# Performance work log

Measured on AMD Instinct MI355X. Metric: run time of the kernel, lower is better.

Reference implementation:

```python
import jax, jax.numpy as jnp
import numpy as np

B, D, C, S = 65536, 128, 10, 2
LAMBDA_E, LAMBDA_OD = 0.1, 0.036
GAMMA_E, GAMMA_OD = 2.0, 2.0
STEP_SIZE = 1000.0


def setup_inputs() -> dict:
    key = jax.random.key(0)
    ks = jax.random.split(key, 12)
    inp = {
        "mean_t": jax.random.normal(ks[0], (B, D), jnp.float32),
        "mean_s": jax.random.normal(ks[1], (B, D), jnp.float32),
        "log_std_t": jax.random.normal(ks[2], (B, D), jnp.float32),
        "log_std_s": jax.random.normal(ks[3], (B, D), jnp.float32),
        "y_zt": jax.random.normal(ks[4], (B, C), jnp.float32),
        "s_zt": jax.random.normal(ks[5], (B, S), jnp.float32),
        "eps_prior_t": jax.random.normal(ks[6], (B, D), jnp.float32),
        "eps_prior_s": jax.random.normal(ks[7], (B, D), jnp.float32),
        "eps_t": jax.random.normal(ks[8], (B, D), jnp.float32),
        "eps_s": jax.random.normal(ks[9], (B, D), jnp.float32),
        "target": jax.random.randint(ks[10], (B,), 0, C, jnp.int64),
        "current_step": 500,
    }
    return inp


def _kld_batchmean(log_p, t):
    # torch KLDivLoss(reduction='batchmean'): sum(t * (log t - log_p)) / batch
    return jnp.sum(t * (jnp.log(t) - log_p)) / t.shape[0]


def reference(mean_t, mean_s, log_std_t, log_std_s, y_zt, s_zt,
              eps_prior_t, eps_prior_s, eps_t, eps_s, target, current_step):
    # CIFAR10 branch: cross entropy on task logits
    logp_y = jax.nn.log_softmax(y_zt, axis=1)
    L_t = -jnp.mean(jnp.take_along_axis(logp_y, target[:, None], axis=1))

    # entropy loss on sensitive discriminator output
    sm = jax.nn.softmax(s_zt, axis=1)
    lsm = jax.nn.log_softmax(s_zt, axis=1)
    Loss_e = -jnp.sum(sm * lsm) / s_zt.shape[0]

    # prior samples: N(0, I) and N(1, I)  (mean_tensors(zeros, ones))
    prior_t = eps_prior_t            # mean 0
    prior_s = 1.0 + eps_prior_s      # mean 1

    # encoder samples: MVN(mean, diag(exp(log_std))) -> std = exp(0.5*log_std)
    # torch .sample() is non-differentiable -> stop_gradient
    enc_t = jax.lax.stop_gradient(mean_t + jnp.exp(0.5 * log_std_t) * eps_t)
    enc_s = jax.lax.stop_gradient(mean_s + jnp.exp(0.5 * log_std_s) * eps_s)

    L_zt = _kld_batchmean(jax.nn.log_softmax(prior_t, axis=1), jax.nn.softmax(enc_t, axis=1))
    L_zs = _kld_batchmean(jax.nn.log_softmax(prior_s, axis=1), jax.nn.softmax(enc_s, axis=1))

    frac = current_step / STEP_SIZE
    lam_e = LAMBDA_E * GAMMA_E ** frac
    lam_od = LAMBDA_OD * GAMMA_OD ** frac
    return L_t + lam_e * Loss_e + lam_od * (L_zt + L_zs)
```

## Files before the change

### kernel.cpp

```cpp
#include <hip/hip_runtime.h>
#include <hip/hip_bf16.h>
#include <math.h>

#define BATCH   65536
#define NCLS    10
#define NBLOCKS 2048
#define PAIRS   4

typedef float vf4 __attribute__((ext_vector_type(4)));


__global__ __launch_bounds__(256, 4) void crit_main(
    const float* __restrict__ mean_t,      const float* __restrict__ mean_s,
    const float* __restrict__ log_std_t,   const float* __restrict__ log_std_s,
    const float* __restrict__ y_zt,        const float* __restrict__ s_zt,
    const float* __restrict__ eps_prior_t, const float* __restrict__ eps_prior_s,
    const float* __restrict__ eps_t,       const float* __restrict__ eps_s,
    const int*   __restrict__ target,
    double*      __restrict__ ws_partial)
{
    const int tid  = threadIdx.x;
    const int lane = tid & 63;
    const int sub  = lane & 31;
    const int half = lane >> 5;
    const int gwave = blockIdx.x * 4 + (tid >> 6);
    const int base  = gwave * PAIRS;

    const vf4* MT = (const vf4*)mean_t;
    const vf4* LT = (const vf4*)log_std_t;
    const vf4* ET = (const vf4*)eps_t;
    const vf4* PT = (const vf4*)eps_prior_t;
    const vf4* MS = (const vf4*)mean_s;
    const vf4* LS = (const vf4*)log_std_s;
    const vf4* ES = (const vf4*)eps_s;
    const vf4* PS = (const vf4*)eps_prior_s;

    int    tgt[PAIRS];
    float2 y0[PAIRS], y1[PAIRS], y2[PAIRS], y3[PAIRS], y4[PAIRS], s2[PAIRS];
    if (sub == 0) {
        #pragma unroll
        for (int i = 0; i < PAIRS; ++i) {
            const int r = (base + i) * 2 + half;
            tgt[i] = target[r];
            const float* yr = y_zt + (size_t)r * NCLS;
            y0[i] = *(const float2*)(yr + 0);
            y1[i] = *(const float2*)(yr + 2);
            y2[i] = *(const float2*)(yr + 4);
            y3[i] = *(const float2*)(yr + 6);
            y4[i] = *(const float2*)(yr + 8);
            s2[i] = *(const float2*)(s_zt + (size_t)r * 2);
        }
    }

    float part[PAIRS][6];
    #pragma unroll
    for (int i = 0; i < PAIRS; ++i) {
        const int fidx = (base + i) * 64 + lane;

        const vf4 mu_t = __builtin_nontemporal_load(&MT[fidx]);
        const vf4 ls_t = __builtin_nontemporal_load(&LT[fidx]);
        const vf4 ep_t = __builtin_nontemporal_load(&ET[fidx]);
        const vf4 pr_t = __builtin_nontemporal_load(&PT[fidx]);
        const vf4 mu_s = __builtin_nontemporal_load(&MS[fidx]);
        const vf4 ls_s = __builtin_nontemporal_load(&LS[fidx]);
        const vf4 ep_s = __builtin_nontemporal_load(&ES[fidx]);
        const vf4 pr_s = __builtin_nontemporal_load(&PS[fidx]);

        const float et0 = fmaf(__expf(0.5f * ls_t.x), ep_t.x, mu_t.x);
        const float et1 = fmaf(__expf(0.5f * ls_t.y), ep_t.y, mu_t.y);
        const float et2 = fmaf(__expf(0.5f * ls_t.z), ep_t.z, mu_t.z);
        const float et3 = fmaf(__expf(0.5f * ls_t.w), ep_t.w, mu_t.w);
        const float es0 = fmaf(__expf(0.5f * ls_s.x), ep_s.x, mu_s.x);
        const float es1 = fmaf(__expf(0.5f * ls_s.y), ep_s.y, mu_s.y);
        const float es2 = fmaf(__expf(0.5f * ls_s.z), ep_s.z, mu_s.z);
        const float es3 = fmaf(__expf(0.5f * ls_s.w), ep_s.w, mu_s.w);

        const float xt0 = __expf(et0), xt1 = __expf(et1);
        const float xt2 = __expf(et2), xt3 = __expf(et3);
        const float xs0 = __expf(es0), xs1 = __expf(es1);
        const float xs2 = __expf(es2), xs3 = __expf(es3);

        part[i][0] = (xt0 + xt1) + (xt2 + xt3);
        part[i][1] = (__expf(pr_t.x) + __expf(pr_t.y)) + (__expf(pr_t.z) + __expf(pr_t.w));
        part[i][2] = (xt0 * (et0 - pr_t.x) + xt1 * (et1 - pr_t.y))
                   + (xt2 * (et2 - pr_t.z) + xt3 * (et3 - pr_t.w));
        part[i][3] = (xs0 + xs1) + (xs2 + xs3);
        part[i][4] = (__expf(pr_s.x) + __expf(pr_s.y)) + (__expf(pr_s.z) + __expf(pr_s.w));
        part[i][5] = (xs0 * (es0 - pr_s.x) + xs1 * (es1 - pr_s.y))
                   + (xs2 * (es2 - pr_s.z) + xs3 * (es3 - pr_s.w));
    }

    #pragma unroll
    for (int m = 16; m >= 1; m >>= 1) {
        #pragma unroll
        for (int i = 0; i < PAIRS; ++i) {
            #pragma unroll
            for (int j = 0; j < 6; ++j) part[i][j] += __shfl_xor(part[i][j], m, 64);
        }
    }

    float kl_sum = 0.0f, ce_sum = 0.0f, H_sum = 0.0f;
    #pragma unroll
    for (int i = 0; i < PAIRS; ++i) {
        const float rt = 1.0f / part[i][0];
        const float rs = 1.0f / part[i][3];
        kl_sum += part[i][2] * rt + __logf(part[i][1] * rt)
                + part[i][5] * rs + __logf(part[i][4] * rs);
    }
    if (sub == 0) {
        #pragma unroll
        for (int i = 0; i < PAIRS; ++i) {
            const int t = tgt[i];
            float yt = y0[i].x;
            yt = (t == 1) ? y0[i].y : yt;
            yt = (t == 2) ? y1[i].x : yt;
            yt = (t == 3) ? y1[i].y : yt;
            yt = (t == 4) ? y2[i].x : yt;
            yt = (t == 5) ? y2[i].y : yt;
            yt = (t == 6) ? y3[i].x : yt;
            yt = (t == 7) ? y3[i].y : yt;
            yt = (t == 8) ? y4[i].x : yt;
            yt = (t == 9) ? y4[i].y : yt;

            const float Z = (__expf(y0[i].x) + __expf(y0[i].y))
                          + (__expf(y1[i].x) + __expf(y1[i].y))
                          + (__expf(y2[i].x) + __expf(y2[i].y))
                          + (__expf(y3[i].x) + __expf(y3[i].y))
                          + (__expf(y4[i].x) + __expf(y4[i].y));
            ce_sum += __logf(Z) - yt;

            const float za = __expf(s2[i].x), zb = __expf(s2[i].y);
            const float Zs = za + zb;
            const float lses = __logf(Zs);
            H_sum += -((za / Zs) * (s2[i].x - lses) + (zb / Zs) * (s2[i].y - lses));
        }
    }

    __shared__ double sh[8][3];
    if (sub == 0) {
        const int slot = tid >> 5;
        sh[slot][0] = (double)ce_sum;
        sh[slot][1] = (double)H_sum;
        sh[slot][2] = (double)kl_sum;
    }
    __syncthreads();
    if (tid == 0) {
        double c = 0.0, h = 0.0, k = 0.0;
        #pragma unroll
        for (int i = 0; i < 8; ++i) { c += sh[i][0]; h += sh[i][1]; k += sh[i][2]; }
        ws_partial[blockIdx.x * 3 + 0] = c;
        ws_partial[blockIdx.x * 3 + 1] = h;
        ws_partial[blockIdx.x * 3 + 2] = k;
    }
}

__global__ __launch_bounds__(256) void crit_reduce(
    const double* __restrict__ ws_partial,
    const int*    __restrict__ step_ptr,
    float*        __restrict__ out,
    int nblocks)
{
    const int tid = threadIdx.x;
    double c = 0.0, h = 0.0, k = 0.0;
    for (int i = tid; i < nblocks; i += 256) {
        c += ws_partial[3 * i + 0];
        h += ws_partial[3 * i + 1];
        k += ws_partial[3 * i + 2];
    }
    __shared__ double sc[256], sh_[256], sk[256];
    sc[tid] = c; sh_[tid] = h; sk[tid] = k;
    __syncthreads();
    for (int s = 128; s > 0; s >>= 1) {
        if (tid < s) { sc[tid] += sc[tid + s]; sh_[tid] += sh_[tid + s]; sk[tid] += sk[tid + s]; }
        __syncthreads();
    }
    if (tid == 0) {
        double frac  = (double)step_ptr[0] / 1000.0;
        double lam_e  = 0.1   * exp2(frac);
        double lam_od = 0.036 * exp2(frac);
        out[0] = (float)((sc[0] + lam_e * sh_[0] + lam_od * sk[0]) / (double)BATCH);
    }
}

extern "C" void kernel_launch(void* const* d_in, const int* in_sizes, int n_in,
                              void* d_out, int out_size, void* d_ws, size_t ws_size,
                              hipStream_t stream) {
    const float* mean_t      = (const float*)d_in[0];
    const float* mean_s      = (const float*)d_in[1];
    const float* log_std_t   = (const float*)d_in[2];
    const float* log_std_s   = (const float*)d_in[3];
    const float* y_zt        = (const float*)d_in[4];
    const float* s_zt        = (const float*)d_in[5];
    const float* eps_prior_t = (const float*)d_in[6];
    const float* eps_prior_s = (const float*)d_in[7];
    const float* eps_t       = (const float*)d_in[8];
    const float* eps_s       = (const float*)d_in[9];
    const int*   target      = (const int*)d_in[10];
    const int*   step_ptr    = (const int*)d_in[11];

    double* ws_partial = (double*)d_ws;
    float*  out        = (float*)d_out;

    crit_main<<<NBLOCKS, 256, 0, stream>>>(
        mean_t, mean_s, log_std_t, log_std_s, y_zt, s_zt,
        eps_prior_t, eps_prior_s, eps_t, eps_s, target, ws_partial);
    crit_reduce<<<1, 256, 0, stream>>>(ws_partial, step_ptr, out, NBLOCKS);
}
```

Baseline: 243.2 us.

## Split CE/entropy work into dedicated blocks and remap KL rows to 16-lane groups

The per-row cross-entropy and entropy work moves out of the KL blocks into 64 extra dedicated blocks, where every thread handles four rows instead of one lane per half-wave doing it serially. In the KL blocks, each 16-lane group now handles one row with two vf4 loads per tensor, giving 8 rows per wave and a 4-step shuffle reduction instead of 5. The aim is to drop the serialized scalar y_zt/s_zt/target loads and lane divergence from the bandwidth-bound KL path. In exchange, the block reduction becomes a full 256-entry double shared-memory tree with more barriers, and the y_zt row accesses in the new blocks are strided by 40 bytes.

```diff
diff --git a/kernel.cpp b/kernel.cpp
--- a/kernel.cpp
+++ b/kernel.cpp
@@ -2,10 +2,11 @@
 #include <hip/hip_bf16.h>
 #include <math.h>
 
-#define BATCH   65536
-#define NCLS    10
-#define NBLOCKS 2048
-#define PAIRS   4
+#define BATCH 65536
+#define NCLS  10
+#define NKL   2048
+#define NCE   64
+#define NBTOT (NKL + NCE)
 
 typedef float vf4 __attribute__((ext_vector_type(4)));
 
@@ -19,138 +20,140 @@
     const int*   __restrict__ target,
     double*      __restrict__ ws_partial)
 {
-    const int tid  = threadIdx.x;
-    const int lane = tid & 63;
-    const int sub  = lane & 31;
-    const int half = lane >> 5;
-    const int gwave = blockIdx.x * 4 + (tid >> 6);
-    const int base  = gwave * PAIRS;
-
-    const vf4* MT = (const vf4*)mean_t;
-    const vf4* LT = (const vf4*)log_std_t;
-    const vf4* ET = (const vf4*)eps_t;
-    const vf4* PT = (const vf4*)eps_prior_t;
-    const vf4* MS = (const vf4*)mean_s;
-    const vf4* LS = (const vf4*)log_std_s;
-    const vf4* ES = (const vf4*)eps_s;
-    const vf4* PS = (const vf4*)eps_prior_s;
-
-    int    tgt[PAIRS];
-    float2 y0[PAIRS], y1[PAIRS], y2[PAIRS], y3[PAIRS], y4[PAIRS], s2[PAIRS];
-    if (sub == 0) {
+    const int tid = threadIdx.x;
+    double ce_d = 0.0, H_d = 0.0, kl_d = 0.0;
+
+    if (blockIdx.x < NKL) {
+        const int lane = tid & 63;
+        const int sub  = lane & 15;
+        const int grp  = (lane >> 4) & 3;
+        const int gwave = blockIdx.x * 4 + (tid >> 6);
+        const int rowbase = gwave * 8;
+
+        const vf4* MT = (const vf4*)mean_t;
+        const vf4* LT = (const vf4*)log_std_t;
+        const vf4* ET = (const vf4*)eps_t;
+        const vf4* PT = (const vf4*)eps_prior_t;
+        const vf4* MS = (const vf4*)mean_s;
+        const vf4* LS = (const vf4*)log_std_s;
+        const vf4* ES = (const vf4*)eps_s;
+        const vf4* PS = (const vf4*)eps_prior_s;
+
         #pragma unroll
-        for (int i = 0; i < PAIRS; ++i) {
-            const int r = (base + i) * 2 + half;
-            tgt[i] = target[r];
+        for (int k = 0; k < 2; ++k) {
+            const int row = rowbase + k * 4 + grp;
+            const int i0 = row * 32 + sub;
+            const int i1 = i0 + 16;
+
+            const vf4 mt0 = __builtin_nontemporal_load(&MT[i0]);
+            const vf4 mt1 = __builtin_nontemporal_load(&MT[i1]);
+            const vf4 lt0 = __builtin_nontemporal_load(&LT[i0]);
+            const vf4 lt1 = __builtin_nontemporal_load(&LT[i1]);
+            const vf4 et0 = __builtin_nontemporal_load(&ET[i0]);
+            const vf4 et1 = __builtin_nontemporal_load(&ET[i1]);
+            const vf4 pt0 = __builtin_nontemporal_load(&PT[i0]);
+            const vf4 pt1 = __builtin_nontemporal_load(&PT[i1]);
+            const vf4 ms0 = __builtin_nontemporal_load(&MS[i0]);
+            const vf4 ms1 = __builtin_nontemporal_load(&MS[i1]);
+            const vf4 ls0 = __builtin_nontemporal_load(&LS[i0]);
+            const vf4 ls1 = __builtin_nontemporal_load(&LS[i1]);
+            const vf4 es0 = __builtin_nontemporal_load(&ES[i0]);
+            const vf4 es1 = __builtin_nontemporal_load(&ES[i1]);
+            const vf4 ps0 = __builtin_nontemporal_load(&PS[i0]);
+            const vf4 ps1 = __builtin_nontemporal_load(&PS[i1]);
+
+            float red[6] = {0.f, 0.f, 0.f, 0.f, 0.f, 0.f};
+            #pragma unroll
+            for (int e = 0; e < 8; ++e) {
+                const int c = e & 3;
+                const float mu_t = (e < 4) ? mt0[c] : mt1[c];
+                const float lg_t = (e < 4) ? lt0[c] : lt1[c];
+                const float ep_t = (e < 4) ? et0[c] : et1[c];
+                const float pr_t = (e < 4) ? pt0[c] : pt1[c];
+                const float mu_s = (e < 4) ? ms0[c] : ms1[c];
+                const float lg_s = (e < 4) ? ls0[c] : ls1[c];
+                const float ep_s = (e < 4) ? es0[c] : es1[c];
+                const float pr_s = (e < 4) ? ps0[c] : ps1[c];
+
+                const float enc_t = fmaf(__expf(0.5f * lg_t), ep_t, mu_t);
+                const float enc_s = fmaf(__expf(0.5f * lg_s), ep_s, mu_s);
+                const float xt = __expf(enc_t);
+                const float xs = __expf(enc_s);
+                red[0] += xt;
+                red[1] += __expf(pr_t);
+                red[2] += xt * (enc_t - pr_t);
+                red[3] += xs;
+                red[4] += __expf(pr_s);
+                red[5] += xs * (enc_s - pr_s);
+            }
+
+            #pragma unroll
+            for (int m = 8; m >= 1; m >>= 1) {
+                #pragma unroll
+                for (int j = 0; j < 6; ++j) red[j] += __shfl_xor(red[j], m, 64);
+            }
+
+            const float rt = 1.0f / red[0];
+            const float rs = 1.0f / red[3];
+            const float kl = red[2] * rt + __logf(red[1] * rt)
+                           + red[5] * rs + __logf(red[4] * rs);
+            kl_d += (sub == 0) ? (double)kl : 0.0;
+        }
+    } else {
+        const int gtid = (blockIdx.x - NKL) * 256 + tid;
+        #pragma unroll
+        for (int k = 0; k < 4; ++k) {
+            const int r = gtid + k * 16384;
             const float* yr = y_zt + (size_t)r * NCLS;
-            y0[i] = *(const float2*)(yr + 0);
-            y1[i] = *(const float2*)(yr + 2);
-            y2[i] = *(const float2*)(yr + 4);
-            y3[i] = *(const float2*)(yr + 6);
-            y4[i] = *(const float2*)(yr + 8);
-            s2[i] = *(const float2*)(s_zt + (size_t)r * 2);
-        }
-    }
-
-    float part[PAIRS][6];
-    #pragma unroll
-    for (int i = 0; i < PAIRS; ++i) {
-        const int fidx = (base + i) * 64 + lane;
-
-        const vf4 mu_t = __builtin_nontemporal_load(&MT[fidx]);
-        const vf4 ls_t = __builtin_nontemporal_load(&LT[fidx]);
-        const vf4 ep_t = __builtin_nontemporal_load(&ET[fidx]);
-        const vf4 pr_t = __builtin_nontemporal_load(&PT[fidx]);
-        const vf4 mu_s = __builtin_nontemporal_load(&MS[fidx]);
-        const vf4 ls_s = __builtin_nontemporal_load(&LS[fidx]);
-        const vf4 ep_s = __builtin_nontemporal_load(&ES[fidx]);
-        const vf4 pr_s = __builtin_nontemporal_load(&PS[fidx]);
-
-        const float et0 = fmaf(__expf(0.5f * ls_t.x), ep_t.x, mu_t.x);
-        const float et1 = fmaf(__expf(0.5f * ls_t.y), ep_t.y, mu_t.y);
-        const float et2 = fmaf(__expf(0.5f * ls_t.z), ep_t.z, mu_t.z);
-        const float et3 = fmaf(__expf(0.5f * ls_t.w), ep_t.w, mu_t.w);
-        const float es0 = fmaf(__expf(0.5f * ls_s.x), ep_s.x, mu_s.x);
-        const float es1 = fmaf(__expf(0.5f * ls_s.y), ep_s.y, mu_s.y);
-        const float es2 = fmaf(__expf(0.5f * ls_s.z), ep_s.z, mu_s.z);
-        const float es3 = fmaf(__expf(0.5f * ls_s.w), ep_s.w, mu_s.w);
-
-        const float xt0 = __expf(et0), xt1 = __expf(et1);
-        const float xt2 = __expf(et2), xt3 = __expf(et3);
-        const float xs0 = __expf(es0), xs1 = __expf(es1);
-        const float xs2 = __expf(es2), xs3 = __expf(es3);
-
-        part[i][0] = (xt0 + xt1) + (xt2 + xt3);
-        part[i][1] = (__expf(pr_t.x) + __expf(pr_t.y)) + (__expf(pr_t.z) + __expf(pr_t.w));
-        part[i][2] = (xt0 * (et0 - pr_t.x) + xt1 * (et1 - pr_t.y))
-                   + (xt2 * (et2 - pr_t.z) + xt3 * (et3 - pr_t.w));
-        part[i][3] = (xs0 + xs1) + (xs2 + xs3);
-        part[i][4] = (__expf(pr_s.x) + __expf(pr_s.y)) + (__expf(pr_s.z) + __expf(pr_s.w));
-        part[i][5] = (xs0 * (es0 - pr_s.x) + xs1 * (es1 - pr_s.y))
-                   + (xs2 * (es2 - pr_s.z) + xs3 * (es3 - pr_s.w));
-    }
-
-    #pragma unroll
-    for (int m = 16; m >= 1; m >>= 1) {
-        #pragma unroll
-        for (int i = 0; i < PAIRS; ++i) {
-            #pragma unroll
-            for (int j = 0; j < 6; ++j) part[i][j] += __shfl_xor(part[i][j], m, 64);
-        }
-    }
-
-    float kl_sum = 0.0f, ce_sum = 0.0f, H_sum = 0.0f;
-    #pragma unroll
-    for (int i = 0; i < PAIRS; ++i) {
-        const float rt = 1.0f / part[i][0];
-        const float rs = 1.0f / part[i][3];
-        kl_sum += part[i][2] * rt + __logf(part[i][1] * rt)
-                + part[i][5] * rs + __logf(part[i][4] * rs);
-    }
-    if (sub == 0) {
-        #pragma unroll
-        for (int i = 0; i < PAIRS; ++i) {
-            const int t = tgt[i];
-            float yt = y0[i].x;
-            yt = (t == 1) ? y0[i].y : yt;
-            yt = (t == 2) ? y1[i].x : yt;
-            yt = (t == 3) ? y1[i].y : yt;
-            yt = (t == 4) ? y2[i].x : yt;
-            yt = (t == 5) ? y2[i].y : yt;
-            yt = (t == 6) ? y3[i].x : yt;
-            yt = (t == 7) ? y3[i].y : yt;
-            yt = (t == 8) ? y4[i].x : yt;
-            yt = (t == 9) ? y4[i].y : yt;
-
-            const float Z = (__expf(y0[i].x) + __expf(y0[i].y))
-                          + (__expf(y1[i].x) + __expf(y1[i].y))
-                          + (__expf(y2[i].x) + __expf(y2[i].y))
-                          + (__expf(y3[i].x) + __expf(y3[i].y))
-                          + (__expf(y4[i].x) + __expf(y4[i].y));
-            ce_sum += __logf(Z) - yt;
-
-            const float za = __expf(s2[i].x), zb = __expf(s2[i].y);
+            const float2 y0 = *(const float2*)(yr + 0);
+            const float2 y1 = *(const float2*)(yr + 2);
+            const float2 y2 = *(const float2*)(yr + 4);
+            const float2 y3 = *(const float2*)(yr + 6);
+            const float2 y4 = *(const float2*)(yr + 8);
+            const float2 s2 = *(const float2*)(s_zt + (size_t)r * 2);
+            const int    t  = target[r];
+
+            float yt = y0.x;
+            yt = (t == 1) ? y0.y : yt;
+            yt = (t == 2) ? y1.x : yt;
+            yt = (t == 3) ? y1.y : yt;
+            yt = (t == 4) ? y2.x : yt;
+            yt = (t == 5) ? y2.y : yt;
+            yt = (t == 6) ? y3.x : yt;
+            yt = (t == 7) ? y3.y : yt;
+            yt = (t == 8) ? y4.x : yt;
+            yt = (t == 9) ? y4.y : yt;
+
+            const float Z = (__expf(y0.x) + __expf(y0.y))
+                          + (__expf(y1.x) + __expf(y1.y))
+                          + (__expf(y2.x) + __expf(y2.y))
+                          + (__expf(y3.x) + __expf(y3.y))
+                          + (__expf(y4.x) + __expf(y4.y));
+            ce_d += (double)(__logf(Z) - yt);
+
+            const float za = __expf(s2.x), zb = __expf(s2.y);
             const float Zs = za + zb;
             const float lses = __logf(Zs);
-            H_sum += -((za / Zs) * (s2[i].x - lses) + (zb / Zs) * (s2[i].y - lses));
+            H_d += (double)(-((za / Zs) * (s2.x - lses) + (zb / Zs) * (s2.y - lses)));
         }
     }
 
-    __shared__ double sh[8][3];
-    if (sub == 0) {
-        const int slot = tid >> 5;
-        sh[slot][0] = (double)ce_sum;
-        sh[slot][1] = (double)H_sum;
-        sh[slot][2] = (double)kl_sum;
-    }
+    __shared__ double sred[256][3];
+    sred[tid][0] = ce_d; sred[tid][1] = H_d; sred[tid][2] = kl_d;
     __syncthreads();
+    #pragma unroll
+    for (int s = 128; s > 0; s >>= 1) {
+        if (tid < s) {
+            sred[tid][0] += sred[tid + s][0];
+            sred[tid][1] += sred[tid + s][1];
+            sred[tid][2] += sred[tid + s][2];
+        }
+        __syncthreads();
+    }
     if (tid == 0) {
-        double c = 0.0, h = 0.0, k = 0.0;
-        #pragma unroll
-        for (int i = 0; i < 8; ++i) { c += sh[i][0]; h += sh[i][1]; k += sh[i][2]; }
-        ws_partial[blockIdx.x * 3 + 0] = c;
-        ws_partial[blockIdx.x * 3 + 1] = h;
-        ws_partial[blockIdx.x * 3 + 2] = k;
+        ws_partial[blockIdx.x * 3 + 0] = sred[0][0];
+        ws_partial[blockIdx.x * 3 + 1] = sred[0][1];
+        ws_partial[blockIdx.x * 3 + 2] = sred[0][2];
     }
 }
 
@@ -201,8 +204,8 @@
     double* ws_partial = (double*)d_ws;
     float*  out        = (float*)d_out;
 
-    crit_main<<<NBLOCKS, 256, 0, stream>>>(
+    crit_main<<<NBTOT, 256, 0, stream>>>(
         mean_t, mean_s, log_std_t, log_std_s, y_zt, s_zt,
         eps_prior_t, eps_prior_s, eps_t, eps_s, target, ws_partial);
-    crit_reduce<<<1, 256, 0, stream>>>(ws_partial, step_ptr, out, NBLOCKS);
+    crit_reduce<<<1, 256, 0, stream>>>(ws_partial, step_ptr, out, NBTOT);
 }
```

Measured after the change: 239.7 us. Within noise of the previous version (-1.5%).
